# Kernel optimization log

Measured on AMD Instinct MI355X. Metric: run time of the kernel, lower is better.

## Reference

```python
import jax, jax.numpy as jnp
import numpy as np

SMALL_NUMBER = 1e-8
N_NODES = 100000
HIDDEN = 128
N_EDGE_TYPES = 3          # before backward doubling
N_EDGES = 400000          # per edge type
GNN_LAYERS = 8            # shared message/update weights across all 8 steps


def setup_inputs() -> dict:
    key = jax.random.key(0)
    ks = jax.random.split(key, 6)
    scale = 1.0 / np.sqrt(HIDDEN)  # ~xavier for stability
    node_states = jax.random.normal(ks[0], (N_NODES, HIDDEN), dtype=jnp.float32)
    edges = jax.random.randint(ks[1], (N_EDGE_TYPES, N_EDGES, 2), 0, N_NODES, dtype=jnp.int32)
    W_msg = jax.random.normal(ks[2], (2 * N_EDGE_TYPES, HIDDEN, HIDDEN), dtype=jnp.float32) * scale
    b_msg = jnp.zeros((2 * N_EDGE_TYPES, HIDDEN), dtype=jnp.float32)
    w_ih = jax.random.normal(ks[3], (3 * HIDDEN, HIDDEN), dtype=jnp.float32) * scale
    w_hh = jax.random.normal(ks[4], (3 * HIDDEN, HIDDEN), dtype=jnp.float32) * scale
    b_ih = jnp.zeros((3 * HIDDEN,), dtype=jnp.float32)
    b_hh = jnp.zeros((3 * HIDDEN,), dtype=jnp.float32)
    return {"node_states": node_states, "edges": edges, "W_msg": W_msg,
            "b_msg": b_msg, "w_ih": w_ih, "w_hh": w_hh, "b_ih": b_ih, "b_hh": b_hh}


def _message(h, edges_all, W_msg, b_msg):
    # h: [N, D]; edges_all: [E, M, 2]; W_msg: [E, D, D]
    n = h.shape[0]
    # per-edge-type linear transform (== LinearNet(D, D*E) then chunk)
    prop = jnp.einsum('nd,edh->enh', h, W_msg) + b_msg[:, None, :]  # [E, N, D]
    src = edges_all[:, :, 0]  # [E, M]
    tgt = edges_all[:, :, 1]  # [E, M]
    gathered = jax.vmap(lambda p, s: p[s])(prop, src)  # [E, M, D]
    e, m, d = gathered.shape
    msgs = jax.ops.segment_sum(gathered.reshape(e * m, d), tgt.reshape(e * m), num_segments=n)
    counts = jax.ops.segment_sum(jnp.ones((e * m,), dtype=jnp.float32), tgt.reshape(e * m), num_segments=n)
    divisor = jnp.where(counts == 0, 1.0, counts)
    return msgs / divisor[:, None] + SMALL_NUMBER  # mean aggregation as in torch code


def _gru_cell(x, h, w_ih, w_hh, b_ih, b_hh):
    gi = x @ w_ih.T + b_ih  # [N, 3D]
    gh = h @ w_hh.T + b_hh
    ir, iz, inn = jnp.split(gi, 3, axis=1)
    hr, hz, hn = jnp.split(gh, 3, axis=1)
    r = jax.nn.sigmoid(ir + hr)
    z = jax.nn.sigmoid(iz + hz)
    n = jnp.tanh(inn + r * hn)
    return (1.0 - z) * n + z * h


def reference(node_states, edges, W_msg, b_msg, w_ih, w_hh, b_ih, b_hh):
    old_node_states = node_states
    # backward_edges: append flipped edge lists -> 2*E edge types
    edges_all = jnp.concatenate([edges, edges[:, :, ::-1]], axis=0)  # [2E, M, 2]
    h = node_states
    for _ in range(GNN_LAYERS):  # shared weights (weight_sharing == gnn_layers)
        msgs = _message(h, edges_all, W_msg, b_msg)
        h = _gru_cell(msgs, h, w_ih, w_hh, b_ih, b_hh)
    return (h, old_node_states)
```

## Files before the change

kernel.cpp:

```cpp
#include <hip/hip_runtime.h>

#define NN     100000
#define NP     100096
#define HD     128
#define NE     400000
#define TOT    2400000
#define L6     600000
#define NLAYER 8
#define SCHUNK 2048

typedef unsigned short ushort_t;
typedef unsigned int   uint_t;

typedef __bf16 bf16x8 __attribute__((ext_vector_type(8)));
typedef float  f32x4  __attribute__((ext_vector_type(4)));

__device__ __forceinline__ f32x4 mfma16(bf16x8 a, bf16x8 b, f32x4 c) {
  return __builtin_amdgcn_mfma_f32_16x16x32_bf16(a, b, c, 0, 0, 0);
}

__device__ __forceinline__ unsigned short f2bf(float f) {
  unsigned int u = __builtin_bit_cast(unsigned int, f);
  u = (u + 0x7FFFu + ((u >> 16) & 1u)) >> 16;
  return (unsigned short)u;
}
__device__ __forceinline__ float bflo(uint_t v) { return __builtin_bit_cast(float, v << 16); }
__device__ __forceinline__ float bfhi(uint_t v) { return __builtin_bit_cast(float, v & 0xFFFF0000u); }
__device__ __forceinline__ float bf2f(ushort_t v) { return __builtin_bit_cast(float, (uint_t)v << 16); }
__device__ __forceinline__ uint_t packbf(float x, float y) {
  return (uint_t)f2bf(x) | ((uint_t)f2bf(y) << 16);
}

#define GLOAD_LDS16(g, l) __builtin_amdgcn_global_load_lds( \
    (__attribute__((address_space(1))) void*)(g),           \
    (__attribute__((address_space(3))) void*)(l), 16, 0, 0)


__global__ __launch_bounds__(256) void k_init(const float* __restrict__ ns,
    float* __restrict__ oh, float* __restrict__ oold, ushort_t* __restrict__ hbf) {
  int i = blockIdx.x * 256 + threadIdx.x;
  if (i < NN * HD) {
    float v = ns[i];
    oh[i] = v; oold[i] = v; hbf[i] = f2bf(v);
  }
}

__global__ __launch_bounds__(256) void k_prep(const float* __restrict__ Wm,
    const float* __restrict__ wih, const float* __restrict__ whh,
    ushort_t* __restrict__ Wcat, ushort_t* __restrict__ wihb, ushort_t* __restrict__ whhb) {
  int t = blockIdx.x * 256 + threadIdx.x;
  if (t < 128 * 768) {
    int n = t / 768, k = t % 768;
    int e = k >> 7, d = k & 127;
    Wcat[t] = f2bf(Wm[(e * 128 + d) * 128 + n]);
  }
  if (t < 384 * 128) {
    wihb[t] = f2bf(wih[t]);
    whhb[t] = f2bf(whh[t]);
  }
}

__global__ __launch_bounds__(256) void k_hist(const int* __restrict__ edges, int* __restrict__ cnt6) {
  int t = blockIdx.x * 256 + threadIdx.x;
  if (t >= TOT) return;
  int e = t / NE, m = t - e * NE;
  int tgt;
  if (e < 3) tgt = edges[(e * NE + m) * 2 + 1];
  else       tgt = edges[((e - 3) * NE + m) * 2];
  atomicAdd(&cnt6[tgt * 6 + e], 1);
}

__global__ __launch_bounds__(256) void k_div(const int* __restrict__ cnt6,
    float* __restrict__ divf) {
  int i = blockIdx.x * 256 + threadIdx.x;
  if (i < NN) {
    int c = 0;
#pragma unroll
    for (int e = 0; e < 6; e++) c += cnt6[i * 6 + e];
    divf[i] = c ? (float)c : 1.0f;
  }
}

__global__ __launch_bounds__(256) void k_scan1(const int* __restrict__ cnt, int* __restrict__ bsum) {
  int base = blockIdx.x * SCHUNK + threadIdx.x * 8;
  int s = 0;
#pragma unroll
  for (int j = 0; j < 8; j++) { int idx = base + j; s += (idx < L6) ? cnt[idx] : 0; }
  for (int o = 32; o > 0; o >>= 1) s += __shfl_down(s, o);
  __shared__ int sm[4];
  if ((threadIdx.x & 63) == 0) sm[threadIdx.x >> 6] = s;
  __syncthreads();
  if (threadIdx.x == 0) bsum[blockIdx.x] = sm[0] + sm[1] + sm[2] + sm[3];
}

__global__ __launch_bounds__(512) void k_scan2(int* __restrict__ bsum, int nb) {
  int t = threadIdx.x, lane = t & 63, wv = t >> 6;
  int orig = (t < nb) ? bsum[t] : 0;
  int v = orig;
  for (int o = 1; o < 64; o <<= 1) { int x = __shfl_up(v, o); if (lane >= o) v += x; }
  __shared__ int ws[8];
  if (lane == 63) ws[wv] = v;
  __syncthreads();
  int add = 0;
  for (int w = 0; w < wv; w++) add += ws[w];
  if (t < nb) bsum[t] = v - orig + add;
}

__global__ __launch_bounds__(256) void k_scan3(const int* __restrict__ cnt,
    const int* __restrict__ bsum, int* __restrict__ offs) {
  int base = blockIdx.x * SCHUNK + threadIdx.x * 8;
  int vals[8], pre[8];
  int s = 0;
#pragma unroll
  for (int j = 0; j < 8; j++) {
    int idx = base + j;
    vals[j] = (idx < L6) ? cnt[idx] : 0;
    pre[j] = s; s += vals[j];
  }
  int lane = threadIdx.x & 63, wvi = threadIdx.x >> 6;
  int v = s;
  for (int o = 1; o < 64; o <<= 1) { int t = __shfl_up(v, o); if (lane >= o) v += t; }
  __shared__ int wsum[4];
  if (lane == 63) wsum[wvi] = v;
  __syncthreads();
  int wpre = 0;
  for (int w = 0; w < wvi; w++) wpre += wsum[w];
  int texcl = (v - s) + wpre + bsum[blockIdx.x];
#pragma unroll
  for (int j = 0; j < 8; j++) {
    int idx = base + j;
    if (idx < L6) {
      offs[idx] = texcl + pre[j];
      if (idx == L6 - 1) offs[L6] = texcl + pre[j] + vals[j];
    }
  }
}

__global__ __launch_bounds__(256) void k_fill(const int* __restrict__ edges,
    int* __restrict__ cursor6, int* __restrict__ entries) {
  int t = blockIdx.x * 256 + threadIdx.x;
  if (t >= TOT) return;
  int e = t / NE, m = t - e * NE;
  int src, tgt;
  if (e < 3) { int b = (e * NE + m) * 2;       src = edges[b];     tgt = edges[b + 1]; }
  else       { int b = ((e - 3) * NE + m) * 2; src = edges[b + 1]; tgt = edges[b]; }
  int pos = atomicAdd(&cursor6[tgt * 6 + e], 1);
  entries[pos] = src;
}


#define FLUSH() do { switch (curE) {                        \
    case 0: a0x += cx; a0y += cy; break;                    \
    case 1: a1x += cx; a1y += cy; break;                    \
    case 2: a2x += cx; a2y += cy; break;                    \
    case 3: a3x += cx; a3y += cy; break;                    \
    case 4: a4x += cx; a4y += cy; break;                    \
    default: a5x += cx; a5y += cy; break; }                 \
    cx = 0.f; cy = 0.f; } while (0)

#define ADV() do { while (curE < 5 && pos == nextB) {       \
    FLUSH(); curE++;                                        \
    nextB = __builtin_amdgcn_readlane(bj, curE + 1); } } while (0)

__global__ __launch_bounds__(512) void k_agg(const ushort_t* __restrict__ hbf,
    const int* __restrict__ offs6, const int* __restrict__ entries,
    ushort_t* __restrict__ agg, int node0, int rows) {
  int lane = threadIdx.x & 63, wv = threadIdx.x >> 6;
  int row = blockIdx.x * 8 + wv;
  if (row >= rows) return;
  int n = node0 + row;
  float a0x = 0.f, a0y = 0.f, a1x = 0.f, a1y = 0.f, a2x = 0.f, a2y = 0.f;
  float a3x = 0.f, a3y = 0.f, a4x = 0.f, a4y = 0.f, a5x = 0.f, a5y = 0.f;
  if (n < NN) {
    int bj = offs6[n * 6 + (lane < 6 ? lane : 6)];
    int S0 = __builtin_amdgcn_readlane(bj, 0);
    int S6 = __builtin_amdgcn_readlane(bj, 6);
    int deg = S6 - S0;
    int curE = 0;
    int nextB = __builtin_amdgcn_readlane(bj, 1);
    float cx = 0.f, cy = 0.f;
    int pos = S0;
    int voff = lane * 4;
    const char* hb = (const char*)hbf;
    for (int c0 = 0; c0 < deg; c0 += 64) {
      int m = deg - c0; if (m > 64) m = 64;
      int ent = entries[S0 + c0 + (lane < m ? lane : 0)];
      for (int j = 0; j < m; j += 4) {
        int j1 = j + 1 < m ? j + 1 : m - 1;
        int j2 = j + 2 < m ? j + 2 : m - 1;
        int j3 = j + 3 < m ? j + 3 : m - 1;
        int s0_ = __builtin_amdgcn_readlane(ent, j);
        int s1_ = __builtin_amdgcn_readlane(ent, j1);
        int s2_ = __builtin_amdgcn_readlane(ent, j2);
        int s3_ = __builtin_amdgcn_readlane(ent, j3);
        uint_t v0 = *(const uint_t*)(hb + ((size_t)(uint_t)s0_ << 8) + voff);
        uint_t v1 = *(const uint_t*)(hb + ((size_t)(uint_t)s1_ << 8) + voff);
        uint_t v2 = *(const uint_t*)(hb + ((size_t)(uint_t)s2_ << 8) + voff);
        uint_t v3 = *(const uint_t*)(hb + ((size_t)(uint_t)s3_ << 8) + voff);
        ADV(); cx += bflo(v0); cy += bfhi(v0); pos++;
        if (j + 1 < m) { ADV(); cx += bflo(v1); cy += bfhi(v1); pos++; }
        if (j + 2 < m) { ADV(); cx += bflo(v2); cy += bfhi(v2); pos++; }
        if (j + 3 < m) { ADV(); cx += bflo(v3); cy += bfhi(v3); pos++; }
      }
    }
    ADV();
    FLUSH();
  }
  uint_t* outp = (uint_t*)(agg + (size_t)row * 768);
  outp[0 * 64 + lane] = packbf(a0x, a0y);
  outp[1 * 64 + lane] = packbf(a1x, a1y);
  outp[2 * 64 + lane] = packbf(a2x, a2y);
  outp[3 * 64 + lane] = packbf(a3x, a3y);
  outp[4 * 64 + lane] = packbf(a4x, a4y);
  outp[5 * 64 + lane] = packbf(a5x, a5y);
}

__global__ __launch_bounds__(256) void k_gemm1(const ushort_t* __restrict__ agg,
    const ushort_t* __restrict__ Wcat, const int* __restrict__ cnt6,
    const float* __restrict__ divf, const float* __restrict__ b_msg,
    ushort_t* __restrict__ msgs, int node0) {
  __shared__ ushort_t Alds[128 * 64];
  __shared__ ushort_t Blds[128 * 64];
  int lane = threadIdx.x & 63, wv = threadIdx.x >> 6;
  int wr = wv >> 1, wc = wv & 1;
  int rbase = blockIdx.x * 128;
  f32x4 acc[4][4] = {};
  for (int k0 = 0; k0 < 768; k0 += 64) {
#pragma unroll
    for (int i = 0; i < 4; i++) {
      int off = wv * 1024 + i * 4096;
      int loff = off + lane * 16;
      int r2 = loff >> 7, c16 = (loff >> 4) & 7;
      GLOAD_LDS16(agg + (size_t)(rbase + r2) * 768 + k0 + c16 * 8, (char*)Alds + off);
      GLOAD_LDS16(Wcat + (size_t)r2 * 768 + k0 + c16 * 8,          (char*)Blds + off);
    }
    __syncthreads();
#pragma unroll
    for (int kk = 0; kk < 2; kk++) {
      int kb = kk * 64 + ((lane >> 4) << 4);
      bf16x8 af[4], bfv[4];
#pragma unroll
      for (int m = 0; m < 4; m++) {
        af[m]  = *(const bf16x8*)((const char*)Alds + (wr * 64 + m * 16 + (lane & 15)) * 128 + kb);
        bfv[m] = *(const bf16x8*)((const char*)Blds + (wc * 64 + m * 16 + (lane & 15)) * 128 + kb);
      }
#pragma unroll
      for (int m = 0; m < 4; m++)
#pragma unroll
        for (int nf = 0; nf < 4; nf++)
          acc[m][nf] = mfma16(af[m], bfv[nf], acc[m][nf]);
    }
    __syncthreads();
  }
#pragma unroll
  for (int m = 0; m < 4; m++) {
#pragma unroll
    for (int r = 0; r < 4; r++) {
      int node = node0 + rbase + wr * 64 + m * 16 + (lane >> 4) * 4 + r;
      if (node < NN) {
        float dv = divf[node];
        const int* c6 = cnt6 + (size_t)node * 6;
#pragma unroll
        for (int nf = 0; nf < 4; nf++) {
          int col = wc * 64 + nf * 16 + (lane & 15);
          float badd = 0.f;
#pragma unroll
          for (int e = 0; e < 6; e++) badd += (float)c6[e] * b_msg[e * 128 + col];
          float v = (acc[m][nf][r] + badd) / dv + 1e-8f;
          msgs[(size_t)node * HD + col] = f2bf(v);
        }
      }
    }
  }
}

__global__ __launch_bounds__(512) void k_gru(const ushort_t* __restrict__ msgs,
    const ushort_t* __restrict__ hbf, const ushort_t* __restrict__ wihb,
    const ushort_t* __restrict__ whhb, const float* __restrict__ b_ih,
    const float* __restrict__ b_hh, float* __restrict__ hf,
    ushort_t* __restrict__ hbfo, int last) {
  __shared__ ushort_t Am[64 * 128];
  __shared__ ushort_t Ah[64 * 128];
  int lane = threadIdx.x & 63, wv = threadIdx.x >> 6;
  int rbase = blockIdx.x * 64;
#pragma unroll
  for (int i = 0; i < 2; i++) {
    int off = wv * 1024 + i * 8192;
    int loff = off + lane * 16;
    int r2 = loff >> 8, c16 = (loff >> 4) & 15;
    GLOAD_LDS16(msgs + (size_t)(rbase + r2) * HD + c16 * 8, (char*)Am + off);
    GLOAD_LDS16(hbf  + (size_t)(rbase + r2) * HD + c16 * 8, (char*)Ah + off);
  }
  __syncthreads();
  f32x4 acc[4][6] = {};
#pragma unroll
  for (int ks = 0; ks < 4; ks++) {
    int kb = ks * 64 + ((lane >> 4) << 4);
    bf16x8 am[4], ah[4];
#pragma unroll
    for (int m = 0; m < 4; m++) {
      int rb = (m * 16 + (lane & 15)) * 256 + kb;
      am[m] = *(const bf16x8*)((const char*)Am + rb);
      ah[m] = *(const bf16x8*)((const char*)Ah + rb);
    }
    bf16x8 bi[3], bh[3];
#pragma unroll
    for (int g = 0; g < 3; g++) {
      int n = g * 128 + wv * 16 + (lane & 15);
      int ko = ks * 32 + ((lane >> 4) << 3);
      bi[g] = *(const bf16x8*)(wihb + (size_t)n * HD + ko);
      bh[g] = *(const bf16x8*)(whhb + (size_t)n * HD + ko);
    }
#pragma unroll
    for (int m = 0; m < 4; m++) {
#pragma unroll
      for (int g = 0; g < 3; g++) {
        acc[m][g]     = mfma16(am[m], bi[g], acc[m][g]);
        acc[m][3 + g] = mfma16(ah[m], bh[g], acc[m][3 + g]);
      }
    }
  }
  int d = wv * 16 + (lane & 15);
  float bir = b_ih[d],       bhr = b_hh[d];
  float biz = b_ih[128 + d], bhz = b_hh[128 + d];
  float bin = b_ih[256 + d], bhn = b_hh[256 + d];
#pragma unroll
  for (int m = 0; m < 4; m++) {
#pragma unroll
    for (int r = 0; r < 4; r++) {
      int rloc = m * 16 + (lane >> 4) * 4 + r;
      int row = rbase + rloc;
      if (row < NN) {
        float ir = acc[m][0][r], iz = acc[m][1][r], in = acc[m][2][r];
        float hr = acc[m][3][r], hz = acc[m][4][r], hn = acc[m][5][r];
        float rg = 1.f / (1.f + expf(-(ir + hr + bir + bhr)));
        float zg = 1.f / (1.f + expf(-(iz + hz + biz + bhz)));
        float ng = tanhf(in + bin + rg * (hn + bhn));
        float hold = bf2f(Ah[rloc * 128 + d]);
        float o = (1.f - zg) * ng + zg * hold;
        size_t idx = (size_t)row * HD + d;
        hbfo[idx] = f2bf(o);
        if (last) hf[idx] = o;
      }
    }
  }
}


extern "C" void kernel_launch(void* const* d_in, const int* in_sizes, int n_in,
                              void* d_out, int out_size, void* d_ws, size_t ws_size,
                              hipStream_t stream) {
  const float* node_states = (const float*)d_in[0];
  const int*   edges       = (const int*)d_in[1];
  const float* W_msg       = (const float*)d_in[2];
  const float* b_msg       = (const float*)d_in[3];
  const float* w_ih        = (const float*)d_in[4];
  const float* w_hh        = (const float*)d_in[5];
  const float* b_ih        = (const float*)d_in[6];
  const float* b_hh        = (const float*)d_in[7];
  float* out_h   = (float*)d_out;
  float* out_old = out_h + (size_t)NN * HD;

  char* p = (char*)d_ws;
  auto carve = [&](size_t bytes) { char* r = p; p += (bytes + 255) & ~(size_t)255; return r; };
  ushort_t* hbf   = (ushort_t*)carve((size_t)NP * HD * 2);
  ushort_t* msgs  = (ushort_t*)carve((size_t)NP * HD * 2);
  ushort_t* Wcat  = (ushort_t*)carve((size_t)128 * 768 * 2);
  ushort_t* wihb  = (ushort_t*)carve((size_t)384 * 128 * 2);
  ushort_t* whhb  = (ushort_t*)carve((size_t)384 * 128 * 2);
  int*   cnt6     = (int*)carve((size_t)L6 * 4);
  float* divf     = (float*)carve((size_t)NN * 4);
  int*   offs6    = (int*)carve((size_t)(L6 + 1) * 4);
  int*   cursor6  = (int*)carve((size_t)L6 * 4);
  int*   entries  = (int*)carve((size_t)TOT * 4);
  int*   bsum     = (int*)carve(512 * 4);
  size_t used  = (size_t)(p - (char*)d_ws);
  size_t avail = ws_size > used ? ws_size - used : 0;
  size_t chunk_rows = avail / (768 * 2);
  if (chunk_rows > (size_t)NP) chunk_rows = NP;
  chunk_rows &= ~(size_t)127;
  if (chunk_rows < 128) chunk_rows = 128;
  ushort_t* agg = (ushort_t*)p;

  hipMemsetAsync(cnt6, 0, (size_t)L6 * 4, stream);
  hipMemsetAsync(hbf  + (size_t)NN * HD, 0, (size_t)(NP - NN) * HD * 2, stream);
  hipMemsetAsync(msgs + (size_t)NN * HD, 0, (size_t)(NP - NN) * HD * 2, stream);

  k_init<<<(NN * HD + 255) / 256, 256, 0, stream>>>(node_states, out_h, out_old, hbf);
  k_prep<<<(128 * 768 + 255) / 256, 256, 0, stream>>>(W_msg, w_ih, w_hh, Wcat, wihb, whhb);
  k_hist<<<(TOT + 255) / 256, 256, 0, stream>>>(edges, cnt6);
  k_div<<<(NN + 255) / 256, 256, 0, stream>>>(cnt6, divf);
  int nb = (L6 + SCHUNK - 1) / SCHUNK;
  k_scan1<<<nb, 256, 0, stream>>>(cnt6, bsum);
  k_scan2<<<1, 512, 0, stream>>>(bsum, nb);
  k_scan3<<<nb, 256, 0, stream>>>(cnt6, bsum, offs6);
  hipMemcpyAsync(cursor6, offs6, (size_t)L6 * 4, hipMemcpyDeviceToDevice, stream);
  k_fill<<<(TOT + 255) / 256, 256, 0, stream>>>(edges, cursor6, entries);

  for (int L = 0; L < NLAYER; L++) {
    for (size_t n0 = 0; n0 < (size_t)NP; n0 += chunk_rows) {
      int rows = (int)(((size_t)NP - n0) < chunk_rows ? ((size_t)NP - n0) : chunk_rows);
      k_agg<<<(rows + 7) / 8, 512, 0, stream>>>(hbf, offs6, entries, agg, (int)n0, rows);
      k_gemm1<<<rows / 128, 256, 0, stream>>>(agg, Wcat, cnt6, divf, b_msg, msgs, (int)n0);
    }
    k_gru<<<NP / 64, 512, 0, stream>>>(msgs, hbf, wihb, whhb, b_ih, b_hh,
                                       out_h, hbf, L == NLAYER - 1);
  }
}
```

Measured before the change: 2.271 ms.

## Fuse message GEMM with GRU, ping-pong h buffers, bucket edges for CSR build

Merges the message GEMM and GRU kernels into one 512-thread kernel. The normalized messages stay in LDS and feed straight into the GRU GEMMs, which removes the global msgs round trip and one launch per layer. The hidden state is double-buffered so in-place overwrite across chunks is avoided. LDS reads use an XOR swizzle. CSR construction now first buckets edges by 256-node region and then does shared-memory histograms and fills per region, which improves atomic locality. The trade-offs are more LDS per block, fixed bucket capacity (RCAP) assumptions, and more setup kernels.

```diff
diff --git a/kernel.cpp b/kernel.cpp
--- a/kernel.cpp
+++ b/kernel.cpp
@@ -5,9 +5,11 @@
 #define HD     128
 #define NE     400000
 #define TOT    2400000
-#define L6     600000
+#define L6P    (NP * 6)
 #define NLAYER 8
 #define SCHUNK 2048
+#define NREG   391
+#define RCAP   8192
 
 typedef unsigned short ushort_t;
 typedef unsigned int   uint_t;
@@ -60,20 +62,43 @@
   }
 }
 
-__global__ __launch_bounds__(256) void k_hist(const int* __restrict__ edges, int* __restrict__ cnt6) {
+__global__ __launch_bounds__(256) void k_bucket(const int* __restrict__ edges,
+    int* __restrict__ rcur, int* __restrict__ rbuf) {
   int t = blockIdx.x * 256 + threadIdx.x;
   if (t >= TOT) return;
   int e = t / NE, m = t - e * NE;
-  int tgt;
-  if (e < 3) tgt = edges[(e * NE + m) * 2 + 1];
-  else       tgt = edges[((e - 3) * NE + m) * 2];
-  atomicAdd(&cnt6[tgt * 6 + e], 1);
+  int src, tgt;
+  if (e < 3) { int b = (e * NE + m) * 2;       src = edges[b];     tgt = edges[b + 1]; }
+  else       { int b = ((e - 3) * NE + m) * 2; src = edges[b + 1]; tgt = edges[b]; }
+  int R = tgt >> 8;
+  int pos = atomicAdd(&rcur[R], 1);
+  rbuf[(size_t)R * RCAP + pos] = src | (e << 17) | ((tgt & 255) << 20);
+}
+
+__global__ __launch_bounds__(256) void k_hist2(const int* __restrict__ rcur,
+    const int* __restrict__ rbuf, int* __restrict__ cnt6) {
+  __shared__ int hist[1536];
+  int R = blockIdx.x;
+#pragma unroll
+  for (int j = 0; j < 6; j++) hist[threadIdx.x + j * 256] = 0;
+  __syncthreads();
+  int n = rcur[R];
+  for (int i = threadIdx.x; i < n; i += 256) {
+    int v = rbuf[(size_t)R * RCAP + i];
+    atomicAdd(&hist[((v >> 20) & 255) * 6 + ((v >> 17) & 7)], 1);
+  }
+  __syncthreads();
+#pragma unroll
+  for (int j = 0; j < 6; j++) {
+    int idx = threadIdx.x + j * 256;
+    cnt6[(size_t)R * 1536 + idx] = hist[idx];
+  }
 }
 
 __global__ __launch_bounds__(256) void k_div(const int* __restrict__ cnt6,
     float* __restrict__ divf) {
   int i = blockIdx.x * 256 + threadIdx.x;
-  if (i < NN) {
+  if (i < NP) {
     int c = 0;
 #pragma unroll
     for (int e = 0; e < 6; e++) c += cnt6[i * 6 + e];
@@ -85,7 +110,7 @@
   int base = blockIdx.x * SCHUNK + threadIdx.x * 8;
   int s = 0;
 #pragma unroll
-  for (int j = 0; j < 8; j++) { int idx = base + j; s += (idx < L6) ? cnt[idx] : 0; }
+  for (int j = 0; j < 8; j++) { int idx = base + j; s += (idx < L6P) ? cnt[idx] : 0; }
   for (int o = 32; o > 0; o >>= 1) s += __shfl_down(s, o);
   __shared__ int sm[4];
   if ((threadIdx.x & 63) == 0) sm[threadIdx.x >> 6] = s;
@@ -114,7 +139,7 @@
 #pragma unroll
   for (int j = 0; j < 8; j++) {
     int idx = base + j;
-    vals[j] = (idx < L6) ? cnt[idx] : 0;
+    vals[j] = (idx < L6P) ? cnt[idx] : 0;
     pre[j] = s; s += vals[j];
   }
   int lane = threadIdx.x & 63, wvi = threadIdx.x >> 6;
@@ -129,23 +154,23 @@
 #pragma unroll
   for (int j = 0; j < 8; j++) {
     int idx = base + j;
-    if (idx < L6) {
+    if (idx < L6P) {
       offs[idx] = texcl + pre[j];
-      if (idx == L6 - 1) offs[L6] = texcl + pre[j] + vals[j];
-    }
-  }
-}
-
-__global__ __launch_bounds__(256) void k_fill(const int* __restrict__ edges,
-    int* __restrict__ cursor6, int* __restrict__ entries) {
-  int t = blockIdx.x * 256 + threadIdx.x;
-  if (t >= TOT) return;
-  int e = t / NE, m = t - e * NE;
-  int src, tgt;
-  if (e < 3) { int b = (e * NE + m) * 2;       src = edges[b];     tgt = edges[b + 1]; }
-  else       { int b = ((e - 3) * NE + m) * 2; src = edges[b + 1]; tgt = edges[b]; }
-  int pos = atomicAdd(&cursor6[tgt * 6 + e], 1);
-  entries[pos] = src;
+      if (idx == L6P - 1) offs[L6P] = texcl + pre[j] + vals[j];
+    }
+  }
+}
+
+__global__ __launch_bounds__(256) void k_fill2(const int* __restrict__ rcur,
+    const int* __restrict__ rbuf, int* __restrict__ cursor6, int* __restrict__ entries) {
+  int R = blockIdx.x;
+  int n = rcur[R];
+  for (int i = threadIdx.x; i < n; i += 256) {
+    int v = rbuf[(size_t)R * RCAP + i];
+    int tgt = (R << 8) + ((v >> 20) & 255);
+    int pos = atomicAdd(&cursor6[(size_t)tgt * 6 + ((v >> 17) & 7)], 1);
+    entries[pos] = v & 0x1FFFF;
+  }
 }
 
 
@@ -215,132 +240,143 @@
   outp[5 * 64 + lane] = packbf(a5x, a5y);
 }
 
-__global__ __launch_bounds__(256) void k_gemm1(const ushort_t* __restrict__ agg,
-    const ushort_t* __restrict__ Wcat, const int* __restrict__ cnt6,
-    const float* __restrict__ divf, const float* __restrict__ b_msg,
-    ushort_t* __restrict__ msgs, int node0) {
-  __shared__ ushort_t Alds[128 * 64];
-  __shared__ ushort_t Blds[128 * 64];
+__global__ __launch_bounds__(512, 4) void k_fused(
+    const ushort_t* __restrict__ agg, const ushort_t* __restrict__ Wcat,
+    const int* __restrict__ cnt6, const float* __restrict__ divf,
+    const float* __restrict__ b_msg, const ushort_t* __restrict__ hbfin,
+    const ushort_t* __restrict__ wihb, const ushort_t* __restrict__ whhb,
+    const float* __restrict__ b_ih, const float* __restrict__ b_hh,
+    float* __restrict__ hf, ushort_t* __restrict__ hbfout,
+    int node0, int last) {
+  __shared__ char smem[65536];
+  char* Alds = smem;
+  char* Blds = smem + 16384;
+  char* Mlds = smem + 32768;
+  char* Hlds = smem;
   int lane = threadIdx.x & 63, wv = threadIdx.x >> 6;
   int wr = wv >> 1, wc = wv & 1;
   int rbase = blockIdx.x * 128;
-  f32x4 acc[4][4] = {};
+
+  f32x4 acc[2][4] = {};
   for (int k0 = 0; k0 < 768; k0 += 64) {
 #pragma unroll
-    for (int i = 0; i < 4; i++) {
-      int off = wv * 1024 + i * 4096;
-      int loff = off + lane * 16;
-      int r2 = loff >> 7, c16 = (loff >> 4) & 7;
-      GLOAD_LDS16(agg + (size_t)(rbase + r2) * 768 + k0 + c16 * 8, (char*)Alds + off);
-      GLOAD_LDS16(Wcat + (size_t)r2 * 768 + k0 + c16 * 8,          (char*)Blds + off);
+    for (int i = 0; i < 2; i++) {
+      int base = i * 8192 + wv * 1024;
+      int q = base + lane * 16;
+      int row = q >> 7;
+      int colb = (q & 127) ^ ((row & 7) << 4);
+      GLOAD_LDS16(agg + (size_t)(rbase + row) * 768 + k0 + (colb >> 1), Alds + base);
+      GLOAD_LDS16(Wcat + (size_t)row * 768 + k0 + (colb >> 1), Blds + base);
     }
     __syncthreads();
 #pragma unroll
     for (int kk = 0; kk < 2; kk++) {
-      int kb = kk * 64 + ((lane >> 4) << 4);
-      bf16x8 af[4], bfv[4];
-#pragma unroll
-      for (int m = 0; m < 4; m++) {
-        af[m]  = *(const bf16x8*)((const char*)Alds + (wr * 64 + m * 16 + (lane & 15)) * 128 + kb);
-        bfv[m] = *(const bf16x8*)((const char*)Blds + (wc * 64 + m * 16 + (lane & 15)) * 128 + kb);
-      }
-#pragma unroll
-      for (int m = 0; m < 4; m++)
+      bf16x8 af[2], bv[4];
+#pragma unroll
+      for (int m = 0; m < 2; m++) {
+        int row = wr * 32 + m * 16 + (lane & 15);
+        int b = ((row << 7) + kk * 64 + ((lane >> 4) << 4)) ^ ((row & 7) << 4);
+        af[m] = *(const bf16x8*)(Alds + b);
+      }
+#pragma unroll
+      for (int nf = 0; nf < 4; nf++) {
+        int row = wc * 64 + nf * 16 + (lane & 15);
+        int b = ((row << 7) + kk * 64 + ((lane >> 4) << 4)) ^ ((row & 7) << 4);
+        bv[nf] = *(const bf16x8*)(Blds + b);
+      }
+#pragma unroll
+      for (int m = 0; m < 2; m++)
 #pragma unroll
         for (int nf = 0; nf < 4; nf++)
-          acc[m][nf] = mfma16(af[m], bfv[nf], acc[m][nf]);
+          acc[m][nf] = mfma16(af[m], bv[nf], acc[m][nf]);
     }
     __syncthreads();
   }
 #pragma unroll
-  for (int m = 0; m < 4; m++) {
+  for (int i = 0; i < 4; i++) {
+    int base = i * 8192 + wv * 1024;
+    int q = base + lane * 16;
+    int row = q >> 8;
+    int colb = (q & 255) ^ ((row & 7) << 4);
+    GLOAD_LDS16(hbfin + (size_t)(node0 + rbase + row) * HD + (colb >> 1), Hlds + base);
+  }
+#pragma unroll
+  for (int m = 0; m < 2; m++) {
 #pragma unroll
     for (int r = 0; r < 4; r++) {
-      int node = node0 + rbase + wr * 64 + m * 16 + (lane >> 4) * 4 + r;
-      if (node < NN) {
-        float dv = divf[node];
-        const int* c6 = cnt6 + (size_t)node * 6;
-#pragma unroll
-        for (int nf = 0; nf < 4; nf++) {
-          int col = wc * 64 + nf * 16 + (lane & 15);
-          float badd = 0.f;
-#pragma unroll
-          for (int e = 0; e < 6; e++) badd += (float)c6[e] * b_msg[e * 128 + col];
-          float v = (acc[m][nf][r] + badd) / dv + 1e-8f;
-          msgs[(size_t)node * HD + col] = f2bf(v);
-        }
-      }
-    }
-  }
-}
-
-__global__ __launch_bounds__(512) void k_gru(const ushort_t* __restrict__ msgs,
-    const ushort_t* __restrict__ hbf, const ushort_t* __restrict__ wihb,
-    const ushort_t* __restrict__ whhb, const float* __restrict__ b_ih,
-    const float* __restrict__ b_hh, float* __restrict__ hf,
-    ushort_t* __restrict__ hbfo, int last) {
-  __shared__ ushort_t Am[64 * 128];
-  __shared__ ushort_t Ah[64 * 128];
-  int lane = threadIdx.x & 63, wv = threadIdx.x >> 6;
-  int rbase = blockIdx.x * 64;
-#pragma unroll
-  for (int i = 0; i < 2; i++) {
-    int off = wv * 1024 + i * 8192;
-    int loff = off + lane * 16;
-    int r2 = loff >> 8, c16 = (loff >> 4) & 15;
-    GLOAD_LDS16(msgs + (size_t)(rbase + r2) * HD + c16 * 8, (char*)Am + off);
-    GLOAD_LDS16(hbf  + (size_t)(rbase + r2) * HD + c16 * 8, (char*)Ah + off);
-  }
-  __syncthreads();
-  f32x4 acc[4][6] = {};
-#pragma unroll
-  for (int ks = 0; ks < 4; ks++) {
-    int kb = ks * 64 + ((lane >> 4) << 4);
-    bf16x8 am[4], ah[4];
-#pragma unroll
-    for (int m = 0; m < 4; m++) {
-      int rb = (m * 16 + (lane & 15)) * 256 + kb;
-      am[m] = *(const bf16x8*)((const char*)Am + rb);
-      ah[m] = *(const bf16x8*)((const char*)Ah + rb);
-    }
-    bf16x8 bi[3], bh[3];
-#pragma unroll
-    for (int g = 0; g < 3; g++) {
-      int n = g * 128 + wv * 16 + (lane & 15);
-      int ko = ks * 32 + ((lane >> 4) << 3);
-      bi[g] = *(const bf16x8*)(wihb + (size_t)n * HD + ko);
-      bh[g] = *(const bf16x8*)(whhb + (size_t)n * HD + ko);
-    }
-#pragma unroll
-    for (int m = 0; m < 4; m++) {
-#pragma unroll
-      for (int g = 0; g < 3; g++) {
-        acc[m][g]     = mfma16(am[m], bi[g], acc[m][g]);
-        acc[m][3 + g] = mfma16(ah[m], bh[g], acc[m][3 + g]);
-      }
-    }
-  }
+      int rloc = wr * 32 + m * 16 + (lane >> 4) * 4 + r;
+      int node = node0 + rbase + rloc;
+      float dv = divf[node];
+      const int* c6 = cnt6 + (size_t)node * 6;
+      int c[6];
+#pragma unroll
+      for (int e = 0; e < 6; e++) c[e] = c6[e];
+#pragma unroll
+      for (int nf = 0; nf < 4; nf++) {
+        int col = wc * 64 + nf * 16 + (lane & 15);
+        float badd = 0.f;
+#pragma unroll
+        for (int e = 0; e < 6; e++) badd += (float)c[e] * b_msg[e * 128 + col];
+        float v = (acc[m][nf][r] + badd) / dv + 1e-8f;
+        int b = ((rloc << 8) + col * 2) ^ ((rloc & 7) << 4);
+        *(ushort_t*)(Mlds + b) = f2bf(v);
+      }
+    }
+  }
+  __syncthreads();
+
   int d = wv * 16 + (lane & 15);
   float bir = b_ih[d],       bhr = b_hh[d];
   float biz = b_ih[128 + d], bhz = b_hh[128 + d];
   float bin = b_ih[256 + d], bhn = b_hh[256 + d];
 #pragma unroll
-  for (int m = 0; m < 4; m++) {
-#pragma unroll
-    for (int r = 0; r < 4; r++) {
-      int rloc = m * 16 + (lane >> 4) * 4 + r;
-      int row = rbase + rloc;
-      if (row < NN) {
-        float ir = acc[m][0][r], iz = acc[m][1][r], in = acc[m][2][r];
-        float hr = acc[m][3][r], hz = acc[m][4][r], hn = acc[m][5][r];
-        float rg = 1.f / (1.f + expf(-(ir + hr + bir + bhr)));
-        float zg = 1.f / (1.f + expf(-(iz + hz + biz + bhz)));
-        float ng = tanhf(in + bin + rg * (hn + bhn));
-        float hold = bf2f(Ah[rloc * 128 + d]);
-        float o = (1.f - zg) * ng + zg * hold;
-        size_t idx = (size_t)row * HD + d;
-        hbfo[idx] = f2bf(o);
-        if (last) hf[idx] = o;
+  for (int rd = 0; rd < 4; rd++) {
+    f32x4 acb[2][6] = {};
+#pragma unroll
+    for (int ks = 0; ks < 4; ks++) {
+      bf16x8 am[2], ah[2];
+#pragma unroll
+      for (int m = 0; m < 2; m++) {
+        int row = rd * 32 + m * 16 + (lane & 15);
+        int b = ((row << 8) + ks * 64 + ((lane >> 4) << 4)) ^ ((row & 7) << 4);
+        am[m] = *(const bf16x8*)(Mlds + b);
+        ah[m] = *(const bf16x8*)(Hlds + b);
+      }
+      bf16x8 bi[3], bh[3];
+#pragma unroll
+      for (int g = 0; g < 3; g++) {
+        int nidx = g * 128 + d;
+        int ko = ks * 32 + ((lane >> 4) << 3);
+        bi[g] = *(const bf16x8*)(wihb + (size_t)nidx * HD + ko);
+        bh[g] = *(const bf16x8*)(whhb + (size_t)nidx * HD + ko);
+      }
+#pragma unroll
+      for (int m = 0; m < 2; m++)
+#pragma unroll
+        for (int g = 0; g < 3; g++) {
+          acb[m][g]     = mfma16(am[m], bi[g], acb[m][g]);
+          acb[m][3 + g] = mfma16(ah[m], bh[g], acb[m][3 + g]);
+        }
+    }
+#pragma unroll
+    for (int m = 0; m < 2; m++) {
+#pragma unroll
+      for (int r = 0; r < 4; r++) {
+        int rloc = rd * 32 + m * 16 + (lane >> 4) * 4 + r;
+        int row = node0 + rbase + rloc;
+        if (row < NN) {
+          float ir = acb[m][0][r], iz = acb[m][1][r], in = acb[m][2][r];
+          float hr = acb[m][3][r], hz = acb[m][4][r], hn = acb[m][5][r];
+          float rg = 1.f / (1.f + expf(-(ir + hr + bir + bhr)));
+          float zg = 1.f / (1.f + expf(-(iz + hz + biz + bhz)));
+          float ng = tanhf(in + bin + rg * (hn + bhn));
+          int hb = ((rloc << 8) + d * 2) ^ ((rloc & 7) << 4);
+          float hold = bf2f(*(const ushort_t*)(Hlds + hb));
+          float o = (1.f - zg) * ng + zg * hold;
+          size_t idx = (size_t)row * HD + d;
+          hbfout[idx] = f2bf(o);
+          if (last) hf[idx] = o;
+        }
       }
     }
   }
@@ -363,17 +399,19 @@
 
   char* p = (char*)d_ws;
   auto carve = [&](size_t bytes) { char* r = p; p += (bytes + 255) & ~(size_t)255; return r; };
-  ushort_t* hbf   = (ushort_t*)carve((size_t)NP * HD * 2);
-  ushort_t* msgs  = (ushort_t*)carve((size_t)NP * HD * 2);
+  ushort_t* hbfA  = (ushort_t*)carve((size_t)NP * HD * 2);
+  ushort_t* hbfB  = (ushort_t*)carve((size_t)NP * HD * 2);
   ushort_t* Wcat  = (ushort_t*)carve((size_t)128 * 768 * 2);
   ushort_t* wihb  = (ushort_t*)carve((size_t)384 * 128 * 2);
   ushort_t* whhb  = (ushort_t*)carve((size_t)384 * 128 * 2);
-  int*   cnt6     = (int*)carve((size_t)L6 * 4);
-  float* divf     = (float*)carve((size_t)NN * 4);
-  int*   offs6    = (int*)carve((size_t)(L6 + 1) * 4);
-  int*   cursor6  = (int*)carve((size_t)L6 * 4);
+  int*   cnt6     = (int*)carve((size_t)L6P * 4);
+  float* divf     = (float*)carve((size_t)NP * 4);
+  int*   offs6    = (int*)carve((size_t)(L6P + 1) * 4);
+  int*   cursor6  = (int*)carve((size_t)L6P * 4);
   int*   entries  = (int*)carve((size_t)TOT * 4);
   int*   bsum     = (int*)carve(512 * 4);
+  int*   rcur     = (int*)carve((size_t)NREG * 4);
+  int*   rbuf     = (int*)carve((size_t)NREG * RCAP * 4);
   size_t used  = (size_t)(p - (char*)d_ws);
   size_t avail = ws_size > used ? ws_size - used : 0;
   size_t chunk_rows = avail / (768 * 2);
@@ -382,28 +420,33 @@
   if (chunk_rows < 128) chunk_rows = 128;
   ushort_t* agg = (ushort_t*)p;
 
-  hipMemsetAsync(cnt6, 0, (size_t)L6 * 4, stream);
-  hipMemsetAsync(hbf  + (size_t)NN * HD, 0, (size_t)(NP - NN) * HD * 2, stream);
-  hipMemsetAsync(msgs + (size_t)NN * HD, 0, (size_t)(NP - NN) * HD * 2, stream);
-
-  k_init<<<(NN * HD + 255) / 256, 256, 0, stream>>>(node_states, out_h, out_old, hbf);
+  hipMemsetAsync(rcur, 0, (size_t)NREG * 4, stream);
+  hipMemsetAsync(hbfA + (size_t)NN * HD, 0, (size_t)(NP - NN) * HD * 2, stream);
+  hipMemsetAsync(hbfB + (size_t)NN * HD, 0, (size_t)(NP - NN) * HD * 2, stream);
+
+  k_init<<<(NN * HD + 255) / 256, 256, 0, stream>>>(node_states, out_h, out_old, hbfA);
   k_prep<<<(128 * 768 + 255) / 256, 256, 0, stream>>>(W_msg, w_ih, w_hh, Wcat, wihb, whhb);
-  k_hist<<<(TOT + 255) / 256, 256, 0, stream>>>(edges, cnt6);
-  k_div<<<(NN + 255) / 256, 256, 0, stream>>>(cnt6, divf);
-  int nb = (L6 + SCHUNK - 1) / SCHUNK;
+  k_bucket<<<(TOT + 255) / 256, 256, 0, stream>>>(edges, rcur, rbuf);
+  k_hist2<<<NREG, 256, 0, stream>>>(rcur, rbuf, cnt6);
+  k_div<<<(NP + 255) / 256, 256, 0, stream>>>(cnt6, divf);
+  int nb = (L6P + SCHUNK - 1) / SCHUNK;
   k_scan1<<<nb, 256, 0, stream>>>(cnt6, bsum);
   k_scan2<<<1, 512, 0, stream>>>(bsum, nb);
   k_scan3<<<nb, 256, 0, stream>>>(cnt6, bsum, offs6);
-  hipMemcpyAsync(cursor6, offs6, (size_t)L6 * 4, hipMemcpyDeviceToDevice, stream);
-  k_fill<<<(TOT + 255) / 256, 256, 0, stream>>>(edges, cursor6, entries);
-
+  hipMemcpyAsync(cursor6, offs6, (size_t)L6P * 4, hipMemcpyDeviceToDevice, stream);
+  k_fill2<<<NREG, 256, 0, stream>>>(rcur, rbuf, cursor6, entries);
+
+  ushort_t* hA = hbfA;
+  ushort_t* hB = hbfB;
   for (int L = 0; L < NLAYER; L++) {
+    int last = (L == NLAYER - 1);
     for (size_t n0 = 0; n0 < (size_t)NP; n0 += chunk_rows) {
       int rows = (int)(((size_t)NP - n0) < chunk_rows ? ((size_t)NP - n0) : chunk_rows);
-      k_agg<<<(rows + 7) / 8, 512, 0, stream>>>(hbf, offs6, entries, agg, (int)n0, rows);
-      k_gemm1<<<rows / 128, 256, 0, stream>>>(agg, Wcat, cnt6, divf, b_msg, msgs, (int)n0);
-    }
-    k_gru<<<NP / 64, 512, 0, stream>>>(msgs, hbf, wihb, whhb, b_ih, b_hh,
-                                       out_h, hbf, L == NLAYER - 1);
-  }
-}
+      k_agg<<<(rows + 7) / 8, 512, 0, stream>>>(hA, offs6, entries, agg, (int)n0, rows);
+      k_fused<<<rows / 128, 512, 0, stream>>>(agg, Wcat, cnt6, divf, b_msg, hA,
+                                              wihb, whhb, b_ih, b_hh,
+                                              out_h, hB, (int)n0, last);
+    }
+    ushort_t* tmp = hA; hA = hB; hB = tmp;
+  }
+}
```

Measured after the change: 3.280 ms, median of 3. 1.44x slower.
